# Performance work log

Hardware: AMD Instinct MI355X
Metric: run time of the kernel (lower is better)

The kernel has to match this reference:

```python
import jax, jax.numpy as jnp
import numpy as np

N, MAXO, IN_DIM = 4096, 16, 512
RNN_UNITS = (512, 512)
COMM_UNITS = (512, 256)
SIG = COMM_UNITS[-1]
COMM_IN = SIG + 5 + RNN_UNITS[-1]  # signal + one-hot(4) + dist + tiled features


def _lstm(x, h, c, Wx, Wh, b):
    # Keras LSTMCell gate order: i, f, g(candidate), o
    z = x @ Wx + h @ Wh + b
    i, f, g, o = jnp.split(z, 4, axis=-1)
    c2 = jax.nn.sigmoid(f) * c + jax.nn.sigmoid(i) * jnp.tanh(g)
    h2 = jax.nn.sigmoid(o) * jnp.tanh(c2)
    return h2, c2


def _mk_lstm(key, in_dim, units, scale=0.05):
    k1, k2, k3 = jax.random.split(key, 3)
    Wx = scale * jax.random.normal(k1, (in_dim, 4 * units), dtype=jnp.float32)
    Wh = scale * jax.random.normal(k2, (units, 4 * units), dtype=jnp.float32)
    b = scale * jax.random.normal(k3, (4 * units,), dtype=jnp.float32)
    return Wx, Wh, b


def setup_inputs():
    key = jax.random.key(0)
    ks = jax.random.split(key, 18)
    inputs = jax.random.normal(ks[0], (N, IN_DIM), dtype=jnp.float32)
    # interleaved triples (agent_id in [-1,N), dist, dir in [0,4))
    ids = jax.random.randint(ks[1], (N, MAXO), -1, N)
    dists = jax.random.randint(ks[2], (N, MAXO), 0, 20)
    dirs = jax.random.randint(ks[3], (N, MAXO), 0, 4)
    present_indices = jnp.stack([ids, dists, dirs], axis=2).reshape(N, 3 * MAXO).astype(jnp.int32)

    s = lambda k, shape: 0.05 * jax.random.normal(k, shape, dtype=jnp.float32)
    inp = dict(
        inputs=inputs, present_indices=present_indices,
        rnn_h1=s(ks[4], (N, RNN_UNITS[0])), rnn_c1=s(ks[5], (N, RNN_UNITS[0])),
        rnn_h2=s(ks[6], (N, RNN_UNITS[1])), rnn_c2=s(ks[7], (N, RNN_UNITS[1])),
        comm_h1=s(ks[8], (N, COMM_UNITS[0])), comm_c1=s(ks[9], (N, COMM_UNITS[0])),
        comm_h2=s(ks[10], (N, COMM_UNITS[1])), comm_c2=s(ks[11], (N, COMM_UNITS[1])),
        signals=s(ks[12], (N, SIG)),
    )
    inp['Wx1'], inp['Wh1'], inp['b1'] = _mk_lstm(ks[13], IN_DIM, RNN_UNITS[0])
    inp['Wx2'], inp['Wh2'], inp['b2'] = _mk_lstm(ks[14], RNN_UNITS[0], RNN_UNITS[1])
    inp['CWx1'], inp['CWh1'], inp['Cb1'] = _mk_lstm(ks[15], COMM_IN, COMM_UNITS[0])
    inp['CWx2'], inp['CWh2'], inp['Cb2'] = _mk_lstm(ks[16], COMM_UNITS[0], COMM_UNITS[1])
    return inp


def _forward(inputs, present_indices,
             rnn_h1, rnn_c1, rnn_h2, rnn_c2,
             comm_h1, comm_c1, comm_h2, comm_c2, signals,
             Wx1, Wh1, b1, Wx2, Wh2, b2,
             CWx1, CWh1, Cb1, CWx2, CWh2, Cb2):
    n = inputs.shape[0]
    # inner stacked LSTM step; features = output of last layer
    h1, c1 = _lstm(inputs, rnn_h1, rnn_c1, Wx1, Wh1, b1)
    h2, c2 = _lstm(h1, rnn_h2, rnn_c2, Wx2, Wh2, b2)
    features = h2  # [n, RNN_UNITS[-1]]

    vis_dists = present_indices[:, 1::3].astype(jnp.float32)      # [n, MAXO]
    vis_dirs = present_indices[:, 2::3]                            # [n, MAXO]
    pres = present_indices[:, 0::3]                                # [n, MAXO]
    dirs_onehot = jax.nn.one_hot(vis_dirs, 4, dtype=jnp.float32)   # [n, MAXO, 4]

    # append self at the end of the neighbor sequence
    pres = jnp.concatenate([pres, jnp.arange(n, dtype=pres.dtype)[:, None]], axis=1)  # [n, T]
    vis_dists = jnp.pad(vis_dists, ((0, 0), (0, 1)))
    dirs_onehot = jnp.pad(dirs_onehot, ((0, 0), (0, 1), (0, 0)))

    # _gather_present: zero row for absent (-1) neighbors
    padded_signals = jnp.pad(signals, ((1, 0), (0, 0)))            # [n+1, SIG]
    gathered = padded_signals[pres + 1]                            # [n, T, SIG]
    mask = pres >= 0                                               # [n, T]

    T = pres.shape[1]
    sig_in = jnp.concatenate([
        gathered,
        dirs_onehot,
        vis_dists[:, :, None],
        jnp.broadcast_to(features[:, None, :], (n, T, features.shape[-1])),
    ], axis=2)                                                     # [n, T, COMM_IN]

    # masked stacked-LSTM scan over the neighbor axis (Keras RNN mask semantics:
    # masked steps carry states and previous output through)
    xs = (jnp.swapaxes(sig_in, 0, 1), jnp.swapaxes(mask, 0, 1))

    def step(carry, xm):
        ch1, cc1, ch2, cc2, lo = carry
        xt, mt = xm
        nh1, nc1 = _lstm(xt, ch1, cc1, CWx1, CWh1, Cb1)
        nh2, nc2 = _lstm(nh1, ch2, cc2, CWx2, CWh2, Cb2)
        m = mt[:, None]
        carry = (jnp.where(m, nh1, ch1), jnp.where(m, nc1, cc1),
                 jnp.where(m, nh2, ch2), jnp.where(m, nc2, cc2),
                 jnp.where(m, nh2, lo))
        return carry, None

    init = (comm_h1, comm_c1, comm_h2, comm_c2, jnp.zeros_like(comm_h2))
    (nch1, ncc1, nch2, ncc2, out_signals), _ = jax.lax.scan(step, init, xs)

    full_output = jnp.concatenate([out_signals, out_signals, features], axis=1)
    return full_output


def reference(inputs, present_indices,
              rnn_h1, rnn_c1, rnn_h2, rnn_c2,
              comm_h1, comm_c1, comm_h2, comm_c2, signals,
              Wx1, Wh1, b1, Wx2, Wh2, b2,
              CWx1, CWh1, Cb1, CWx2, CWh2, Cb2):
    return _forward(inputs, present_indices,
                    rnn_h1, rnn_c1, rnn_h2, rnn_c2,
                    comm_h1, comm_c1, comm_h2, comm_c2, signals,
                    Wx1, Wh1, b1, Wx2, Wh2, b2,
                    CWx1, CWh1, Cb1, CWx2, CWh2, Cb2)
```

## Files before the change

### kernel.cpp

```cpp
#include <hip/hip_runtime.h>
#include <initializer_list>
#include <cstdint>
#include <cstddef>


typedef short short8 __attribute__((ext_vector_type(8)));
typedef float f32x4 __attribute__((ext_vector_type(4)));
typedef unsigned short us;

#define N_AG 4096

__device__ __forceinline__ us f2bf(float x) {
  unsigned int u = __float_as_uint(x);
  unsigned int r = (u + 0x7fffu + ((u >> 16) & 1u)) >> 16;
  return (us)r;
}
__device__ __forceinline__ float sigm(float x) { return 1.f / (1.f + __expf(-x)); }
__device__ __forceinline__ float tanh_f(float x) {
  float e = __expf(2.f * x);
  return 1.f - 2.f / (1.f + e);
}

struct Pair { const us* A; const us* B; int K; };
struct GemmArgs {
  Pair pr[2]; int np; int N; int nunits;
  const float* bias;
  const float* base2;
  const float* cin;
  float* cout;
  const float* hold;
  float* hout;
  us* hb;
  us* nhb;
  const int* pres; int tt;
  float* C; int mode;
};

typedef __attribute__((address_space(1))) const unsigned int as1u;
typedef __attribute__((address_space(3))) unsigned int as3u;
__device__ __forceinline__ void gload16(const void* g, void* l) {
  __builtin_amdgcn_global_load_lds((as1u*)g, (as3u*)l, 16, 0, 0);
}

__global__ __launch_bounds__(256) void k_gemm(GemmArgs g) {
  __shared__ __align__(16) us lA[128 * 64];
  __shared__ __align__(16) us lB[128 * 64];
  const int t = threadIdx.x;
  const int w = t >> 6, l = t & 63;
  const int bm = blockIdx.y, bn = blockIdx.x;
  const int wm = w & 1, wn = w >> 1;
  const int fr = l & 15, ks = l >> 4;
  f32x4 acc[4][4] = {};

  for (int p = 0; p < g.np; ++p) {
    const us* A = g.pr[p].A;
    const us* B = g.pr[p].B;
    const int K = g.pr[p].K;
    const us* Ab = A + (size_t)bm * 128 * K;
    const us* Bb = B + (size_t)bn * 128 * K;
    for (int k0 = 0; k0 < K; k0 += 64) {
      __syncthreads();
#pragma unroll
      for (int r0 = 0; r0 < 4; ++r0) {
        const int srow = r0 * 32 + (t >> 3);
        const int sslot = (t & 7) ^ (srow & 7);
        gload16(Ab + (size_t)srow * K + k0 + sslot * 8, (char*)lA + r0 * 4096 + w * 1024);
        gload16(Bb + (size_t)srow * K + k0 + sslot * 8, (char*)lB + r0 * 4096 + w * 1024);
      }
      __syncthreads();
#pragma unroll
      for (int kh = 0; kh < 2; ++kh) {
        short8 af[4], bf[4];
#pragma unroll
        for (int mi = 0; mi < 4; ++mi) {
          const int row = wm * 64 + mi * 16 + fr;
          const int s = kh * 4 + ks;
          af[mi] = *(const short8*)((const char*)lA + row * 128 + ((s ^ (row & 7)) << 4));
        }
#pragma unroll
        for (int ni = 0; ni < 4; ++ni) {
          const int row = wn * 64 + ni * 16 + fr;
          const int s = kh * 4 + ks;
          bf[ni] = *(const short8*)((const char*)lB + row * 128 + ((s ^ (row & 7)) << 4));
        }
#pragma unroll
        for (int mi = 0; mi < 4; ++mi)
#pragma unroll
          for (int ni = 0; ni < 4; ++ni)
            acc[mi][ni] = __builtin_amdgcn_mfma_f32_16x16x32_bf16(af[mi], bf[ni], acc[mi][ni], 0, 0, 0);
      }
    }
  }

  const int N = g.N, nu = g.nunits;
  const int u = (bn * 2 + wn) * 16 + fr;
  if (g.mode == 0) {
#pragma unroll
    for (int mi = 0; mi < 4; ++mi)
#pragma unroll
      for (int ni = 0; ni < 4; ++ni)
#pragma unroll
        for (int rr = 0; rr < 4; ++rr) {
          const int grow = bm * 128 + wm * 64 + mi * 16 + ks * 4 + rr;
          const int col = bn * 128 + wn * 64 + ni * 16 + fr;
          g.C[(size_t)grow * N + col] = acc[mi][ni][rr] + g.bias[ni * nu + u];
        }
    return;
  }
  float bi = 0.f, bfg = 0.f, bg = 0.f, bo = 0.f;
  if (!g.base2) { bi = g.bias[u]; bfg = g.bias[nu + u]; bg = g.bias[2 * nu + u]; bo = g.bias[3 * nu + u]; }
#pragma unroll
  for (int mi = 0; mi < 4; ++mi) {
#pragma unroll
    for (int rr = 0; rr < 4; ++rr) {
      const int grow = bm * 128 + wm * 64 + mi * 16 + ks * 4 + rr;
      float zi = acc[mi][0][rr], zf = acc[mi][1][rr], zg = acc[mi][2][rr], zo = acc[mi][3][rr];
      if (g.base2) {
        const float* fb = g.base2 + (size_t)grow * N + bn * 128 + wn * 64 + fr;
        zi += fb[0]; zf += fb[16]; zg += fb[32]; zo += fb[48];
      } else {
        zi += bi; zf += bfg; zg += bg; zo += bo;
      }
      const size_t off = (size_t)grow * nu + u;
      const float cold = g.cin[off];
      const float nc = sigm(zf) * cold + sigm(zi) * tanh_f(zg);
      const float nh = sigm(zo) * tanh_f(nc);
      bool m = true;
      if (g.tt >= 0 && g.tt < 16) m = (g.pres[grow * 48 + 3 * g.tt] >= 0);
      const float cn = m ? nc : cold;
      float hn = nh;
      if (g.hold) hn = m ? nh : g.hold[off];
      if (g.cout) g.cout[off] = cn;
      if (g.hout) g.hout[off] = hn;
      g.hb[off] = f2bf(hn);
      if (g.nhb) g.nhb[off] = f2bf(nh);
    }
  }
}

__global__ __launch_bounds__(256) void k_transpose(const float* __restrict__ src,
    int Nout, int nunits, int Kreal, int Kpad, int roff, us* __restrict__ dst) {
  int idx = blockIdx.x * 256 + threadIdx.x;
  if (idx >= Nout * Kpad) return;
  int col = idx % Nout;
  int k = idx / Nout;
  int gate = (col >> 4) & 3;
  int u = ((col >> 6) << 4) | (col & 15);
  float v = (k < Kreal) ? src[(size_t)(roff + k) * Nout + gate * nunits + u] : 0.f;
  dst[(size_t)col * Kpad + k] = f2bf(v);
}

__global__ __launch_bounds__(256) void k_split(const float* __restrict__ src, int n,
    float* __restrict__ f, us* __restrict__ b) {
  int idx = blockIdx.x * 256 + threadIdx.x;
  if (idx >= n) return;
  float v = src[idx];
  if (f) f[idx] = v;
  if (b) b[idx] = f2bf(v);
}

__global__ __launch_bounds__(256) void k_xvar(const int* __restrict__ pi,
    const float* __restrict__ sig, int t, us* __restrict__ xb) {
  int idx = blockIdx.x * 256 + threadIdx.x;
  if (idx >= N_AG * 320) return;
  int n = idx / 320, c = idx - n * 320;
  float v = 0.f;
  if (t < 16) {
    int p = pi[n * 48 + 3 * t];
    if (c < 256) v = (p >= 0) ? sig[(size_t)p * 256 + c] : 0.f;
    else if (c < 260) v = ((c - 256) == pi[n * 48 + 3 * t + 2]) ? 1.f : 0.f;
    else if (c == 260) v = (float)pi[n * 48 + 3 * t + 1];
  } else {
    if (c < 256) v = sig[(size_t)n * 256 + c];
  }
  xb[idx] = f2bf(v);
}

__global__ __launch_bounds__(256) void k_out(const float* __restrict__ h2,
    const float* __restrict__ feat, float* __restrict__ out) {
  int idx = blockIdx.x * 256 + threadIdx.x;
  if (idx >= N_AG * 1024) return;
  int n = idx >> 10, cc = idx & 1023;
  out[idx] = (cc < 512) ? h2[(size_t)n * 256 + (cc & 255)] : feat[(size_t)n * 512 + cc - 512];
}

extern "C" void kernel_launch(void* const* d_in, const int* in_sizes, int n_in,
                              void* d_out, int out_size, void* d_ws, size_t ws_size,
                              hipStream_t stream) {
  const float* inputs  = (const float*)d_in[0];
  const int*   pres    = (const int*)d_in[1];
  const float* rnn_h1  = (const float*)d_in[2];
  const float* rnn_c1  = (const float*)d_in[3];
  const float* rnn_h2  = (const float*)d_in[4];
  const float* rnn_c2  = (const float*)d_in[5];
  const float* comm_h1 = (const float*)d_in[6];
  const float* comm_c1 = (const float*)d_in[7];
  const float* comm_h2 = (const float*)d_in[8];
  const float* comm_c2 = (const float*)d_in[9];
  const float* signals = (const float*)d_in[10];
  const float* Wx1 = (const float*)d_in[11];
  const float* Wh1 = (const float*)d_in[12];
  const float* b1  = (const float*)d_in[13];
  const float* Wx2 = (const float*)d_in[14];
  const float* Wh2 = (const float*)d_in[15];
  const float* b2  = (const float*)d_in[16];
  const float* CWx1 = (const float*)d_in[17];
  const float* CWh1 = (const float*)d_in[18];
  const float* Cb1  = (const float*)d_in[19];
  const float* CWx2 = (const float*)d_in[20];
  const float* CWh2 = (const float*)d_in[21];
  const float* Cb2  = (const float*)d_in[22];
  float* out = (float*)d_out;
  (void)in_sizes; (void)n_in; (void)out_size;

  char* wsb = (char*)d_ws;
  size_t off = 0;
  auto alloc = [&](size_t bytes) -> char* {
    char* p = wsb + off;
    off = (off + bytes + 255) & ~(size_t)255;
    return p;
  };
  us* wx1t  = (us*)alloc(2048 * 512 * 2);
  us* wh1t  = (us*)alloc(2048 * 512 * 2);
  us* wx2t  = (us*)alloc(2048 * 512 * 2);
  us* wh2t  = (us*)alloc(2048 * 512 * 2);
  us* cx1vt = (us*)alloc(2048 * 320 * 2);
  us* cx1ft = (us*)alloc(2048 * 512 * 2);
  us* ch1t  = (us*)alloc(2048 * 512 * 2);
  us* cx2t  = (us*)alloc(1024 * 512 * 2);
  us* ch2t  = (us*)alloc(1024 * 256 * 2);
  us* in_b   = (us*)alloc(4096 * 512 * 2);
  us* rh1_b  = (us*)alloc(4096 * 512 * 2);
  us* rh2_b  = (us*)alloc(4096 * 512 * 2);
  us* h1p_b  = (us*)alloc(4096 * 512 * 2);
  us* ft_b   = (us*)alloc(4096 * 512 * 2);
  us* h1b0   = (us*)alloc(4096 * 512 * 2);
  us* h1b1   = (us*)alloc(4096 * 512 * 2);
  us* nh1_b  = (us*)alloc(4096 * 512 * 2);
  us* h2b0   = (us*)alloc(4096 * 256 * 2);
  us* h2b1   = (us*)alloc(4096 * 256 * 2);
  us* xv_b   = (us*)alloc(4096 * 320 * 2);
  float* feat = (float*)alloc(4096 * 512 * 4);
  float* F1   = (float*)alloc((size_t)4096 * 2048 * 4);
  float* h1 = (float*)alloc(4096 * 512 * 4);
  float* c1 = (float*)alloc(4096 * 512 * 4);
  float* h2 = (float*)alloc(4096 * 256 * 4);
  float* c2 = (float*)alloc(4096 * 256 * 4);
  if (off > ws_size) return;

  auto tsp = [&](const float* src, int Nout, int Kreal, int Kpad, int roff, us* dst) {
    int tot = Nout * Kpad;
    k_transpose<<<dim3((tot + 255) / 256), dim3(256), 0, stream>>>(src, Nout, Nout / 4, Kreal, Kpad, roff, dst);
  };
  tsp(Wx1, 2048, 512, 512, 0, wx1t);
  tsp(Wh1, 2048, 512, 512, 0, wh1t);
  tsp(Wx2, 2048, 512, 512, 0, wx2t);
  tsp(Wh2, 2048, 512, 512, 0, wh2t);
  tsp(CWx1, 2048, 261, 320, 0, cx1vt);
  tsp(CWx1, 2048, 512, 512, 261, cx1ft);
  tsp(CWh1, 2048, 512, 512, 0, ch1t);
  tsp(CWx2, 1024, 512, 512, 0, cx2t);
  tsp(CWh2, 1024, 256, 256, 0, ch2t);

  auto spl = [&](const float* src, int n, float* f, us* b) {
    k_split<<<dim3((n + 255) / 256), dim3(256), 0, stream>>>(src, n, f, b);
  };
  spl(inputs, 4096 * 512, nullptr, in_b);
  spl(rnn_h1, 4096 * 512, nullptr, rh1_b);
  spl(rnn_h2, 4096 * 512, nullptr, rh2_b);
  spl(comm_h1, 4096 * 512, h1, h1b0);
  spl(comm_c1, 4096 * 512, c1, nullptr);
  spl(comm_h2, 4096 * 256, h2, h2b0);
  spl(comm_c2, 4096 * 256, c2, nullptr);

  auto launch = [&](GemmArgs& ga) {
    k_gemm<<<dim3(ga.N / 128, 4096 / 128), dim3(256), 0, stream>>>(ga);
  };
  auto lstm = [&](std::initializer_list<Pair> ps, int Ncols, const float* bias, const float* base2,
                  const float* cin, float* cout, const float* hold, float* hout,
                  us* hb, us* nhb, const int* pm, int tt) {
    GemmArgs ga{};
    int i = 0;
    for (auto& p : ps) ga.pr[i++] = p;
    ga.np = i; ga.N = Ncols; ga.nunits = Ncols / 4;
    ga.bias = bias; ga.base2 = base2; ga.cin = cin; ga.cout = cout;
    ga.hold = hold; ga.hout = hout; ga.hb = hb; ga.nhb = nhb;
    ga.pres = pm; ga.tt = tt; ga.C = nullptr; ga.mode = 1;
    launch(ga);
  };
  auto plain = [&](std::initializer_list<Pair> ps, int Ncols, const float* bias, float* C) {
    GemmArgs ga{};
    int i = 0;
    for (auto& p : ps) ga.pr[i++] = p;
    ga.np = i; ga.N = Ncols; ga.nunits = Ncols / 4;
    ga.bias = bias; ga.C = C; ga.mode = 0; ga.tt = -1;
    launch(ga);
  };

  lstm({{in_b, wx1t, 512}, {rh1_b, wh1t, 512}}, 2048, b1, nullptr,
       rnn_c1, nullptr, nullptr, nullptr, h1p_b, nullptr, nullptr, -1);
  lstm({{h1p_b, wx2t, 512}, {rh2_b, wh2t, 512}}, 2048, b2, nullptr,
       rnn_c2, nullptr, nullptr, feat, ft_b, nullptr, nullptr, -1);
  plain({{ft_b, cx1ft, 512}}, 2048, Cb1, F1);

  us* h1bp[2] = {h1b0, h1b1};
  us* h2bp[2] = {h2b0, h2b1};
  for (int t = 0; t < 17; ++t) {
    const int rd = t & 1, wr = rd ^ 1;
    k_xvar<<<dim3((4096 * 320 + 255) / 256), dim3(256), 0, stream>>>(pres, signals, t, xv_b);
    lstm({{xv_b, cx1vt, 320}, {h1bp[rd], ch1t, 512}}, 2048, nullptr, F1,
         c1, c1, h1, h1, h1bp[wr], nh1_b, pres, t);
    lstm({{nh1_b, cx2t, 512}, {h2bp[rd], ch2t, 256}}, 1024, Cb2, nullptr,
         c2, c2, h2, h2, h2bp[wr], nullptr, pres, t);
  }
  k_out<<<dim3(4096 * 1024 / 256), dim3(256), 0, stream>>>(h2, feat, out);
}
```

Measured before the change: 1.504 ms.

## Double-buffer LDS tiles in GEMM to overlap global loads with MFMA

The GEMM kernel now keeps two LDS buffers for A and B and flattens the loop over operand pairs and K-tiles into one iteration space. The next tile is prefetched into the alternate buffer while MFMAs run on the current one, which leaves one barrier per iteration instead of two. The aim is to hide global-to-LDS latency. In exchange, LDS use doubles to 64KB per block, which may lower occupancy, and the flattened loop assumes at most two pairs.

```diff
diff --git a/kernel.cpp b/kernel.cpp
--- a/kernel.cpp
+++ b/kernel.cpp
@@ -43,8 +43,8 @@
 }
 
 __global__ __launch_bounds__(256) void k_gemm(GemmArgs g) {
-  __shared__ __align__(16) us lA[128 * 64];
-  __shared__ __align__(16) us lB[128 * 64];
+  __shared__ __align__(16) us lA[2][128 * 64];
+  __shared__ __align__(16) us lB[2][128 * 64];
   const int t = threadIdx.x;
   const int w = t >> 6, l = t & 63;
   const int bm = blockIdx.y, bn = blockIdx.x;
@@ -52,44 +52,52 @@
   const int fr = l & 15, ks = l >> 4;
   f32x4 acc[4][4] = {};
 
-  for (int p = 0; p < g.np; ++p) {
-    const us* A = g.pr[p].A;
-    const us* B = g.pr[p].B;
+  const int nk0 = g.pr[0].K >> 6;
+  const int nt = nk0 + ((g.np > 1) ? (g.pr[1].K >> 6) : 0);
+
+  auto stage = [&](int i, int buf) {
+    const int p = (i < nk0) ? 0 : 1;
+    const int kk = ((i < nk0) ? i : i - nk0) << 6;
     const int K = g.pr[p].K;
-    const us* Ab = A + (size_t)bm * 128 * K;
-    const us* Bb = B + (size_t)bn * 128 * K;
-    for (int k0 = 0; k0 < K; k0 += 64) {
-      __syncthreads();
-#pragma unroll
-      for (int r0 = 0; r0 < 4; ++r0) {
-        const int srow = r0 * 32 + (t >> 3);
-        const int sslot = (t & 7) ^ (srow & 7);
-        gload16(Ab + (size_t)srow * K + k0 + sslot * 8, (char*)lA + r0 * 4096 + w * 1024);
-        gload16(Bb + (size_t)srow * K + k0 + sslot * 8, (char*)lB + r0 * 4096 + w * 1024);
+    const us* Ab = g.pr[p].A + (size_t)bm * 128 * K;
+    const us* Bb = g.pr[p].B + (size_t)bn * 128 * K;
+#pragma unroll
+    for (int r0 = 0; r0 < 4; ++r0) {
+      const int srow = r0 * 32 + (t >> 3);
+      const int sslot = (t & 7) ^ (srow & 7);
+      gload16(Ab + (size_t)srow * K + kk + sslot * 8, (char*)lA[buf] + r0 * 4096 + w * 1024);
+      gload16(Bb + (size_t)srow * K + kk + sslot * 8, (char*)lB[buf] + r0 * 4096 + w * 1024);
+    }
+  };
+
+  stage(0, 0);
+  __syncthreads();
+  int cur = 0;
+  for (int i = 0; i < nt; ++i) {
+    if (i + 1 < nt) stage(i + 1, cur ^ 1);
+#pragma unroll
+    for (int kh = 0; kh < 2; ++kh) {
+      short8 af[4], bf[4];
+#pragma unroll
+      for (int mi = 0; mi < 4; ++mi) {
+        const int row = wm * 64 + mi * 16 + fr;
+        const int s = kh * 4 + ks;
+        af[mi] = *(const short8*)((const char*)lA[cur] + row * 128 + ((s ^ (row & 7)) << 4));
       }
-      __syncthreads();
-#pragma unroll
-      for (int kh = 0; kh < 2; ++kh) {
-        short8 af[4], bf[4];
-#pragma unroll
-        for (int mi = 0; mi < 4; ++mi) {
-          const int row = wm * 64 + mi * 16 + fr;
-          const int s = kh * 4 + ks;
-          af[mi] = *(const short8*)((const char*)lA + row * 128 + ((s ^ (row & 7)) << 4));
-        }
-#pragma unroll
-        for (int ni = 0; ni < 4; ++ni) {
-          const int row = wn * 64 + ni * 16 + fr;
-          const int s = kh * 4 + ks;
-          bf[ni] = *(const short8*)((const char*)lB + row * 128 + ((s ^ (row & 7)) << 4));
-        }
-#pragma unroll
-        for (int mi = 0; mi < 4; ++mi)
-#pragma unroll
-          for (int ni = 0; ni < 4; ++ni)
-            acc[mi][ni] = __builtin_amdgcn_mfma_f32_16x16x32_bf16(af[mi], bf[ni], acc[mi][ni], 0, 0, 0);
+#pragma unroll
+      for (int ni = 0; ni < 4; ++ni) {
+        const int row = wn * 64 + ni * 16 + fr;
+        const int s = kh * 4 + ks;
+        bf[ni] = *(const short8*)((const char*)lB[cur] + row * 128 + ((s ^ (row & 7)) << 4));
       }
+#pragma unroll
+      for (int mi = 0; mi < 4; ++mi)
+#pragma unroll
+        for (int ni = 0; ni < 4; ++ni)
+          acc[mi][ni] = __builtin_amdgcn_mfma_f32_16x16x32_bf16(af[mi], bf[ni], acc[mi][ni], 0, 0, 0);
     }
+    __syncthreads();
+    cur ^= 1;
   }
 
   const int N = g.N, nu = g.nunits;
```

After: 1.527 ms. No clear change (+1.5%).
